# Optimization experiments

Hardware: AMD Instinct MI355X
Metric: run time of the kernel (lower is better)

## Reference

```python
import jax, jax.numpy as jnp
import numpy as np

H, KV, D, EPS = 16, 8, 128, 1e-6

def _rms(t, w):
    # per-head RMSNorm over last dim, computed in fp32
    t32 = t.astype(jnp.float32)
    return (w * t32 * jax.lax.rsqrt(jnp.mean(t32 * t32, axis=-1, keepdims=True) + EPS)).astype(t.dtype)

def _rotate_half(t):
    h = t.shape[-1] // 2
    return jnp.concatenate([-t[..., h:], t[..., :h]], axis=-1)

def setup_inputs() -> dict:
    key = jax.random.key(0)
    ks = jax.random.split(key, 8)
    B, S, HS = 4, 2048, 2048
    return {
        'x': jax.random.normal(ks[0], (B, S, HS), dtype=jnp.float32),
        'cos': jax.random.uniform(ks[1], (S, D), dtype=jnp.float32),
        'sin': jax.random.uniform(ks[2], (S, D), dtype=jnp.float32),
        'wq': jax.random.normal(ks[3], (H * D, HS), dtype=jnp.float32) * 0.02,
        'wk': jax.random.normal(ks[4], (KV * D, HS), dtype=jnp.float32) * 0.02,
        'wv': jax.random.normal(ks[5], (KV * D, HS), dtype=jnp.float32) * 0.02,
        'wo': jax.random.normal(ks[6], (HS, H * D), dtype=jnp.float32) * 0.02,
        'q_norm_w': jnp.ones((D,), dtype=jnp.float32),
        'k_norm_w': jnp.ones((D,), dtype=jnp.float32),
    }

def reference(x, cos, sin, wq, wk, wv, wo, q_norm_w, k_norm_w):
    B, S, _ = x.shape
    n_rep = H // KV
    # QKV projections (torch Linear: x @ W^T)
    xq = (x @ wq.T).reshape(B, S, H, D)
    xk = (x @ wk.T).reshape(B, S, KV, D)
    xv = (x @ wv.T).reshape(B, S, KV, D)
    # per-head RMSNorm on q/k
    xq = _rms(xq, q_norm_w)
    xk = _rms(xk, k_norm_w)
    # RoPE: cos/sin [S, D] broadcast over batch and heads
    c = cos[None, :, None, :]
    s = sin[None, :, None, :]
    xq = xq * c + _rotate_half(xq) * s
    xk = xk * c + _rotate_half(xk) * s
    # GQA: repeat kv heads, move heads forward -> [B, H, S, D]
    xq = xq.transpose(0, 2, 1, 3)
    xk = jnp.repeat(xk, n_rep, axis=2).transpose(0, 2, 1, 3)
    xv = jnp.repeat(xv, n_rep, axis=2).transpose(0, 2, 1, 3)
    # causal softmax attention
    scores = jnp.einsum('bhqd,bhkd->bhqk', xq, xk) / jnp.sqrt(jnp.float32(D))
    causal = jnp.tril(jnp.ones((S, S), dtype=bool))
    scores = jnp.where(causal, scores, -jnp.inf)
    attn = jax.nn.softmax(scores, axis=-1)
    out = jnp.einsum('bhqk,bhkd->bhqd', attn, xv)
    out = out.transpose(0, 2, 1, 3).reshape(B, S, H * D)
    return out @ wo.T
```

## Files before the change

kernel.cpp:

```cpp
#include <hip/hip_runtime.h>
#include <hip/hip_bf16.h>
#include <stdint.h>

using bf16 = __hip_bfloat16;
typedef __attribute__((ext_vector_type(8))) short bf16x8;
typedef __attribute__((ext_vector_type(4))) float f32x4;
typedef __attribute__((ext_vector_type(8))) unsigned short ushort8;

#define MFMA16(a,b,c) __builtin_amdgcn_mfma_f32_16x16x32_bf16(a,b,c,0,0,0)

static constexpr int Bc = 4, Sc = 2048, HSc = 2048, Hc = 16, KVc = 8, Dc = 128;

__device__ __forceinline__ void gl_lds16(const void* g, void* l) {
  __builtin_amdgcn_global_load_lds((const __attribute__((address_space(1))) uint32_t*)g,
                                   (__attribute__((address_space(3))) uint32_t*)l, 16, 0, 0);
}

__device__ __forceinline__ unsigned short f2bf(float f) {
  bf16 h = __float2bfloat16(f);
  return *reinterpret_cast<unsigned short*>(&h);
}

__global__ __launch_bounds__(256) void cvt_all(const float* __restrict__ x,
                                               const float* __restrict__ wq,
                                               const float* __restrict__ wk,
                                               const float* __restrict__ wv,
                                               const float* __restrict__ wo,
                                               unsigned short* __restrict__ xb,
                                               unsigned short* __restrict__ wqkv,
                                               unsigned short* __restrict__ wob) {
  const int NX = 2097152, NQ = 524288, NK = 262144, NV = 262144, NO = 524288;
  const int T = NX + NQ + NK + NV + NO;
  int stride = gridDim.x * blockDim.x;
  for (int i = blockIdx.x * blockDim.x + threadIdx.x; i < T; i += stride) {
    const float* s;
    unsigned short* d;
    int j = i;
    if (j < NX) { s = x; d = xb; }
    else if ((j -= NX) < NQ) { s = wq; d = wqkv; }
    else if ((j -= NQ) < NK) { s = wk; d = wqkv + (size_t)NQ * 8; }
    else if ((j -= NK) < NV) { s = wv; d = wqkv + (size_t)(NQ + NK) * 8; }
    else { j -= NV; s = wo; d = wob; }
    const float4 a = *(const float4*)(s + (size_t)j * 8);
    const float4 b = *(const float4*)(s + (size_t)j * 8 + 4);
    ushort8 o;
    o[0] = f2bf(a.x); o[1] = f2bf(a.y); o[2] = f2bf(a.z); o[3] = f2bf(a.w);
    o[4] = f2bf(b.x); o[5] = f2bf(b.y); o[6] = f2bf(b.z); o[7] = f2bf(b.w);
    *(ushort8*)(d + (size_t)j * 8) = o;
  }
}

__device__ __forceinline__ void storeC(float* C, size_t i, float v) { C[i] = v; }
__device__ __forceinline__ void storeC(bf16* C, size_t i, float v) { C[i] = __float2bfloat16(v); }


#define LDA_(MI, BUF)                                                          \
  _Pragma("unroll") for (int rf = 0; rf < 4; ++rf)                             \
  _Pragma("unroll") for (int k = 0; k < 2; ++k) {                              \
    const int row_ = (MI * 4 + rf) * 16 + lr;                                  \
    a[rf][k] = *(const bf16x8*)&sA[BUF][wm][row_][((k * 4 + lg) ^ (row_ & 7)) * 8]; \
  }
#define LDB_(NI, BUF, BREG)                                                    \
  _Pragma("unroll") for (int j = 0; j < 2; ++j)                                \
  _Pragma("unroll") for (int k = 0; k < 2; ++k) {                              \
    const int row_ = (bco + NI * 2 + j) * 16 + lr;                             \
    BREG[j][k] = *(const bf16x8*)&sB[BUF][bh][row_][((k * 4 + lg) ^ (row_ & 7)) * 8]; \
  }
#define MM_(MI, NI, BREG)                                                      \
  __builtin_amdgcn_s_setprio(1);                                               \
  _Pragma("unroll") for (int rf = 0; rf < 4; ++rf)                             \
  _Pragma("unroll") for (int j = 0; j < 2; ++j)                                \
  _Pragma("unroll") for (int k = 0; k < 2; ++k)                                \
    acc[MI * 4 + rf][NI * 2 + j] =                                             \
        MFMA16(a[rf][k], BREG[j][k], acc[MI * 4 + rf][NI * 2 + j]);            \
  __builtin_amdgcn_s_setprio(0);
#define BAR_ __builtin_amdgcn_s_barrier();
#define VM4_ asm volatile("s_waitcnt vmcnt(4)" ::: "memory");
#define VM0_ asm volatile("s_waitcnt vmcnt(0)" ::: "memory");

template <typename OUT_T>
__global__ __launch_bounds__(512, 2) void gemm8(const bf16* __restrict__ A,
                                                const bf16* __restrict__ B,
                                                OUT_T* __restrict__ C,
                                                int M, int N, int K,
                                                int gm, int gn, int rbm, int rbn) {
  const int nwg = gridDim.x;
  const int cpx = nwg >> 3;
  const int swz = (blockIdx.x & 7) * cpx + (blockIdx.x >> 3);
  const int rsz = rbm * rbn;
  const int region = swz / rsz, rid = swz % rsz;
  const int regions_n = gn / rbn;
  const int bm = (region / regions_n) * rbm + rid / rbn;
  const int bn = (region % regions_n) * rbn + rid % rbn;

  __shared__ __align__(16) bf16 sA[2][2][128][64];
  __shared__ __align__(16) bf16 sB[2][2][128][64];

  const int tid = threadIdx.x;
  const int lane = tid & 63;
  const int wave = tid >> 6;
  const int wm = wave >> 2;
  const int wn = wave & 3;
  const int lg = lane >> 4, lr = lane & 15;
  const int bh = wn >> 1;
  const int bco = (wn & 1) * 4;

  const int rowA = bm * 256;
  const int colB = bn * 256;
  const int NT = K >> 6;

  f32x4 acc[8][4];
  #pragma unroll
  for (int i = 0; i < 8; ++i)
    #pragma unroll
    for (int j = 0; j < 4; ++j) acc[i][j] = (f32x4){0.f, 0.f, 0.f, 0.f};

  auto stA = [&](int buf, int half, int kt) {
    const bf16* src = A + (size_t)(rowA + half * 128) * K + kt * 64;
    #pragma unroll
    for (int is = 0; is < 2; ++is) {
      int r = is * 64 + (tid >> 3);
      int sl = (tid & 7) ^ (r & 7);
      gl_lds16(src + (size_t)r * K + sl * 8, &sA[buf][half][r][(tid & 7) * 8]);
    }
  };
  auto stB = [&](int buf, int half, int kt) {
    const bf16* src = B + (size_t)(colB + half * 128) * K + kt * 64;
    #pragma unroll
    for (int is = 0; is < 2; ++is) {
      int r = is * 64 + (tid >> 3);
      int sl = (tid & 7) ^ (r & 7);
      gl_lds16(src + (size_t)r * K + sl * 8, &sB[buf][half][r][(tid & 7) * 8]);
    }
  };

  stB(0, 0, 0); stB(0, 1, 0); stA(0, 0, 0); stA(0, 1, 0);
  stB(1, 0, 1); stB(1, 1, 1);
  VM4_
  __builtin_amdgcn_s_barrier();

  for (int t = 0; t < NT; t += 2) {
    const bool lastit = (t + 2 >= NT);
    bf16x8 a[4][2], bl[2][2], br[2][2];
    LDA_(0, 0) LDB_(0, 0, bl)
    stA(1, 0, t + 1);
    BAR_ MM_(0, 0, bl) BAR_
    LDB_(1, 0, br)
    stA(1, 1, t + 1);
    BAR_ MM_(0, 1, br) BAR_
    LDA_(1, 0)
    if (!lastit) stB(0, 0, t + 2);
    BAR_ MM_(1, 0, bl) BAR_
    if (!lastit) stB(0, 1, t + 2);
    BAR_ MM_(1, 1, br)
    if (lastit) { VM0_ } else { VM4_ }
    BAR_
    LDA_(0, 1) LDB_(0, 1, bl)
    if (!lastit) stA(0, 0, t + 2);
    BAR_ MM_(0, 0, bl) BAR_
    LDB_(1, 1, br)
    if (!lastit) stA(0, 1, t + 2);
    BAR_ MM_(0, 1, br) BAR_
    LDA_(1, 1)
    if (t + 3 < NT) stB(1, 0, t + 3);
    BAR_ MM_(1, 0, bl) BAR_
    if (t + 3 < NT) stB(1, 1, t + 3);
    BAR_ MM_(1, 1, br)
    if (!lastit) { VM4_ }
    BAR_
  }

  #pragma unroll
  for (int rf = 0; rf < 8; ++rf)
    #pragma unroll
    for (int cf = 0; cf < 4; ++cf)
      #pragma unroll
      for (int r = 0; r < 4; ++r) {
        size_t row = rowA + wm * 128 + rf * 16 + lg * 4 + r;
        size_t col = colB + wn * 64 + cf * 16 + lr;
        storeC(C, row * (size_t)N + col, acc[rf][cf][r]);
      }
}

__global__ __launch_bounds__(256) void norm_rope(const bf16* __restrict__ qkv,
                                                 const float* __restrict__ cosT,
                                                 const float* __restrict__ sinT,
                                                 const float* __restrict__ qw,
                                                 const float* __restrict__ kw,
                                                 bf16* __restrict__ Qn, bf16* __restrict__ Kn) {
  const int bs = blockIdx.x;
  const int s = bs & (Sc - 1);
  const int b = bs >> 11;
  const int wave = threadIdx.x >> 6, lane = threadIdx.x & 63;
  const float c0 = cosT[(size_t)s * Dc + lane];
  const float c1 = cosT[(size_t)s * Dc + 64 + lane];
  const float s0 = sinT[(size_t)s * Dc + lane];
  const float s1 = sinT[(size_t)s * Dc + 64 + lane];
  const bf16* row = qkv + (size_t)bs * 4096;
  #pragma unroll
  for (int i = 0; i < 6; ++i) {
    int head = wave * 6 + i;
    bool isQ = head < 16;
    int col = head * Dc;
    float x0 = __bfloat162float(row[col + lane]);
    float x1 = __bfloat162float(row[col + 64 + lane]);
    float ss = x0 * x0 + x1 * x1;
    #pragma unroll
    for (int off = 32; off; off >>= 1) ss += __shfl_xor(ss, off);
    float inv = rsqrtf(ss * (1.0f / 128.0f) + 1e-6f);
    const float* w = isQ ? qw : kw;
    float n0 = x0 * inv * w[lane];
    float n1 = x1 * inv * w[lane + 64];
    float o0 = n0 * c0 - n1 * s0;
    float o1 = n1 * c1 + n0 * s1;
    size_t base;
    bf16* dst;
    if (isQ) { base = ((size_t)(b * Hc + head) * Sc + s) * Dc; dst = Qn; }
    else     { base = ((size_t)(b * KVc + (head - 16)) * Sc + s) * Dc; dst = Kn; }
    dst[base + lane] = __float2bfloat16(o0);
    dst[base + 64 + lane] = __float2bfloat16(o1);
  }
}

__global__ __launch_bounds__(256) void v_transpose(const bf16* __restrict__ qkv,
                                                   bf16* __restrict__ Vt) {
  const int s0 = blockIdx.x * 64;
  const int bk = blockIdx.y;
  __shared__ __align__(16) bf16 tile[64][136];
  const int tid = threadIdx.x;
  const size_t srcbase = ((size_t)(bk >> 3) * Sc + s0) * 4096 + 3072 + (size_t)(bk & 7) * Dc;
  #pragma unroll
  for (int it = 0; it < 4; ++it) {
    int idx = it * 256 + tid;
    int r = idx >> 4, ch = idx & 15;
    *(bf16x8*)&tile[r][ch * 8] = *(const bf16x8*)(qkv + srcbase + (size_t)r * 4096 + ch * 8);
  }
  __syncthreads();
  const size_t dstbase = (size_t)bk * Dc * Sc + s0;
  #pragma unroll
  for (int it = 0; it < 4; ++it) {
    int idx = it * 256 + tid;
    int d = idx >> 3, scc = idx & 7;
    bf16x8 o;
    #pragma unroll
    for (int j = 0; j < 8; ++j) o[j] = *(const short*)&tile[scc * 8 + j][d];
    *(bf16x8*)(Vt + dstbase + (size_t)d * Sc + scc * 8) = o;
  }
}

__global__ __launch_bounds__(512, 4) void flash_kernel(const bf16* __restrict__ Qn,
                                                       const bf16* __restrict__ Kn,
                                                       const bf16* __restrict__ Vt,
                                                       bf16* __restrict__ Out) {
  const int qi = 15 - (blockIdx.x >> 6);
  const int bh = blockIdx.x & 63;
  const int q0 = qi * 128;
  const int b = bh >> 4, h = bh & 15;
  const int kv = h >> 1;
  const int tid = threadIdx.x;
  const int wave = tid >> 6, lane = tid & 63;
  const int lg = lane >> 4, lr = lane & 15;
  const int rm = lr & 7;

  __shared__ __align__(16) bf16 sK[64][128];
  __shared__ __align__(16) bf16 sV[128][64];
  __shared__ __align__(16) bf16 sP[8][16][72];

  const int qrow = q0 + wave * 16;
  const bf16* qbase = Qn + ((size_t)(b * Hc + h) * Sc + qrow + lr) * Dc;
  bf16x8 qf[4];
  #pragma unroll
  for (int kk = 0; kk < 4; ++kk) qf[kk] = *(const bf16x8*)(qbase + kk * 32 + lg * 8);

  f32x4 oacc[8];
  #pragma unroll
  for (int i = 0; i < 8; ++i) oacc[i] = (f32x4){0.f, 0.f, 0.f, 0.f};
  float m_run[4], l_run[4];
  #pragma unroll
  for (int r = 0; r < 4; ++r) { m_run[r] = -3.0e38f; l_run[r] = 0.f; }

  const bf16* kb = Kn + ((size_t)(b * KVc + kv) * Sc) * Dc;
  const bf16* vb = Vt + ((size_t)(b * KVc + kv) * Dc) * Sc;
  const float scl = 0.08838834764831845f * 1.4426950408889634f;

  const int nt = 2 * qi + 2;
  for (int t = 0; t < nt; ++t) {
    const int k0 = t * 64;
    #pragma unroll
    for (int it = 0; it < 2; ++it) {
      int idx = it * 512 + tid;
      int r = idx >> 4, ps = idx & 15;
      int ls = ps ^ (r & 7);
      gl_lds16(kb + (size_t)(k0 + r) * Dc + ls * 8, &sK[r][ps * 8]);
    }
    #pragma unroll
    for (int it = 0; it < 2; ++it) {
      int idx = it * 512 + tid;
      int r = idx >> 3, ps = idx & 7;
      int ls = ps ^ (r & 7);
      gl_lds16(vb + (size_t)r * Sc + k0 + ls * 8, &sV[r][ps * 8]);
    }
    __syncthreads();

    float tt[4][4];
    __builtin_amdgcn_s_setprio(1);
    #pragma unroll
    for (int c = 0; c < 4; ++c) {
      f32x4 sacc = (f32x4){0.f, 0.f, 0.f, 0.f};
      #pragma unroll
      for (int kk = 0; kk < 4; ++kk) {
        bf16x8 kf = *(const bf16x8*)&sK[c * 16 + lr][((kk * 4 + lg) ^ rm) * 8];
        sacc = MFMA16(qf[kk], kf, sacc);
      }
      int kg = k0 + c * 16 + lr;
      #pragma unroll
      for (int r = 0; r < 4; ++r) {
        int qg = qrow + lg * 4 + r;
        tt[c][r] = (kg <= qg) ? sacc[r] * scl : -3.0e38f;
      }
    }
    __builtin_amdgcn_s_setprio(0);

    float pmax[4];
    #pragma unroll
    for (int r = 0; r < 4; ++r) {
      float mx = fmaxf(fmaxf(tt[0][r], tt[1][r]), fmaxf(tt[2][r], tt[3][r]));
      mx = fmaxf(mx, __shfl_xor(mx, 1));
      mx = fmaxf(mx, __shfl_xor(mx, 2));
      mx = fmaxf(mx, __shfl_xor(mx, 4));
      mx = fmaxf(mx, __shfl_xor(mx, 8));
      pmax[r] = mx;
    }
    bool grow = (pmax[0] > m_run[0] + 8.f) || (pmax[1] > m_run[1] + 8.f) ||
                (pmax[2] > m_run[2] + 8.f) || (pmax[3] > m_run[3] + 8.f);
    if (__any(grow)) {
      #pragma unroll
      for (int r = 0; r < 4; ++r) {
        float mnew = fmaxf(m_run[r], pmax[r]);
        float alpha = exp2f(m_run[r] - mnew);
        m_run[r] = mnew;
        l_run[r] *= alpha;
        #pragma unroll
        for (int dc = 0; dc < 8; ++dc) oacc[dc][r] *= alpha;
      }
    }
    #pragma unroll
    for (int r = 0; r < 4; ++r) {
      float local = 0.f;
      #pragma unroll
      for (int c = 0; c < 4; ++c) { tt[c][r] = exp2f(tt[c][r] - m_run[r]); local += tt[c][r]; }
      l_run[r] += local;
    }
    #pragma unroll
    for (int c = 0; c < 4; ++c)
      #pragma unroll
      for (int r = 0; r < 4; ++r)
        sP[wave][lg * 4 + r][c * 16 + lr] = __float2bfloat16(tt[c][r]);

    __builtin_amdgcn_s_setprio(1);
    #pragma unroll
    for (int kk2 = 0; kk2 < 2; ++kk2) {
      bf16x8 pf = *(const bf16x8*)&sP[wave][lr][kk2 * 32 + lg * 8];
      #pragma unroll
      for (int dc = 0; dc < 8; ++dc) {
        bf16x8 vf = *(const bf16x8*)&sV[dc * 16 + lr][((kk2 * 4 + lg) ^ rm) * 8];
        oacc[dc] = MFMA16(pf, vf, oacc[dc]);
      }
    }
    __builtin_amdgcn_s_setprio(0);

    __syncthreads();
  }

  #pragma unroll
  for (int r = 0; r < 4; ++r) {
    float l = l_run[r];
    l += __shfl_xor(l, 1);
    l += __shfl_xor(l, 2);
    l += __shfl_xor(l, 4);
    l += __shfl_xor(l, 8);
    l_run[r] = 1.f / l;
  }
  #pragma unroll
  for (int dc = 0; dc < 8; ++dc)
    #pragma unroll
    for (int r = 0; r < 4; ++r) {
      size_t row = (size_t)b * Sc + qrow + lg * 4 + r;
      Out[row * (size_t)(Hc * Dc) + h * Dc + dc * 16 + lr] =
          __float2bfloat16(oacc[dc][r] * l_run[r]);
    }
}

extern "C" void kernel_launch(void* const* d_in, const int* in_sizes, int n_in,
                              void* d_out, int out_size, void* d_ws, size_t ws_size,
                              hipStream_t stream) {
  const float* x    = (const float*)d_in[0];
  const float* cosT = (const float*)d_in[1];
  const float* sinT = (const float*)d_in[2];
  const float* wq   = (const float*)d_in[3];
  const float* wk   = (const float*)d_in[4];
  const float* wv   = (const float*)d_in[5];
  const float* wo   = (const float*)d_in[6];
  const float* qnw  = (const float*)d_in[7];
  const float* knw  = (const float*)d_in[8];
  float* out = (float*)d_out;

  const size_t MB = 1ull << 20;
  char* ws = (char*)d_ws;
  bf16* xb   = (bf16*)(ws + 0);
  bf16* wqkv = (bf16*)(ws + 32 * MB);
  bf16* wob  = (bf16*)(ws + 48 * MB);
  bf16* qkv  = (bf16*)(ws + 56 * MB);
  bf16* Qn   = (bf16*)(ws + 120 * MB);
  bf16* Kn   = (bf16*)(ws + 152 * MB);
  bf16* Vt   = (bf16*)(ws + 168 * MB);
  bf16* attn = (bf16*)(ws + 184 * MB);

  cvt_all<<<2048, 256, 0, stream>>>(x, wq, wk, wv, wo,
                                    (unsigned short*)xb, (unsigned short*)wqkv,
                                    (unsigned short*)wob);

  gemm8<bf16><<<512, 512, 0, stream>>>(xb, wqkv, qkv, 8192, 4096, 2048, 32, 16, 16, 4);
  norm_rope<<<8192, 256, 0, stream>>>(qkv, cosT, sinT, qnw, knw, Qn, Kn);
  v_transpose<<<dim3(32, 32), 256, 0, stream>>>(qkv, Vt);
  flash_kernel<<<1024, 512, 0, stream>>>(Qn, Kn, Vt, attn);
  gemm8<float><<<256, 512, 0, stream>>>(attn, wob, out, 8192, 2048, 2048, 32, 8, 8, 4);
}
```

Before: 384.4 us.

## Prefetch K/V tiles into registers and fold softmax scale into Q

```diff
diff --git a/kernel.cpp b/kernel.cpp
--- a/kernel.cpp
+++ b/kernel.cpp
@@ -52,7 +52,6 @@
 
 __device__ __forceinline__ void storeC(float* C, size_t i, float v) { C[i] = v; }
 __device__ __forceinline__ void storeC(bf16* C, size_t i, float v) { C[i] = __float2bfloat16(v); }
-
 
 #define LDA_(MI, BUF)                                                          \
   _Pragma("unroll") for (int rf = 0; rf < 4; ++rf)                             \
@@ -192,6 +191,7 @@
   const int s = bs & (Sc - 1);
   const int b = bs >> 11;
   const int wave = threadIdx.x >> 6, lane = threadIdx.x & 63;
+  const float QSCL = 0.08838834764831845f * 1.4426950408889634f;
   const float c0 = cosT[(size_t)s * Dc + lane];
   const float c1 = cosT[(size_t)s * Dc + 64 + lane];
   const float s0 = sinT[(size_t)s * Dc + lane];
@@ -213,6 +213,7 @@
     float n1 = x1 * inv * w[lane + 64];
     float o0 = n0 * c0 - n1 * s0;
     float o1 = n1 * c1 + n0 * s1;
+    if (isQ) { o0 *= QSCL; o1 *= QSCL; }
     size_t base;
     bf16* dst;
     if (isQ) { base = ((size_t)(b * Hc + head) * Sc + s) * Dc; dst = Qn; }
@@ -281,26 +282,37 @@
 
   const bf16* kb = Kn + ((size_t)(b * KVc + kv) * Sc) * Dc;
   const bf16* vb = Vt + ((size_t)(b * KVc + kv) * Dc) * Sc;
-  const float scl = 0.08838834764831845f * 1.4426950408889634f;
+
+  const bf16* kp[2]; const bf16* vp[2];
+  bf16* kwp[2]; bf16* vwp[2];
+  #pragma unroll
+  for (int i2 = 0; i2 < 2; ++i2) {
+    int idx = i2 * 512 + tid;
+    int r = idx >> 4, ps = idx & 15;
+    kp[i2] = kb + (size_t)r * Dc + ps * 8;
+    kwp[i2] = &sK[r][(ps ^ (r & 7)) * 8];
+    int r2 = idx >> 3, ps2 = idx & 7;
+    vp[i2] = vb + (size_t)r2 * Sc + ps2 * 8;
+    vwp[i2] = &sV[r2][(ps2 ^ (r2 & 7)) * 8];
+  }
+
+  bf16x8 rk[2], rv[2];
+  #pragma unroll
+  for (int i2 = 0; i2 < 2; ++i2) { rk[i2] = *(const bf16x8*)kp[i2]; rv[i2] = *(const bf16x8*)vp[i2]; }
+  #pragma unroll
+  for (int i2 = 0; i2 < 2; ++i2) { *(bf16x8*)kwp[i2] = rk[i2]; *(bf16x8*)vwp[i2] = rv[i2]; }
+  __syncthreads();
 
   const int nt = 2 * qi + 2;
   for (int t = 0; t < nt; ++t) {
     const int k0 = t * 64;
-    #pragma unroll
-    for (int it = 0; it < 2; ++it) {
-      int idx = it * 512 + tid;
-      int r = idx >> 4, ps = idx & 15;
-      int ls = ps ^ (r & 7);
-      gl_lds16(kb + (size_t)(k0 + r) * Dc + ls * 8, &sK[r][ps * 8]);
-    }
-    #pragma unroll
-    for (int it = 0; it < 2; ++it) {
-      int idx = it * 512 + tid;
-      int r = idx >> 3, ps = idx & 7;
-      int ls = ps ^ (r & 7);
-      gl_lds16(vb + (size_t)r * Sc + k0 + ls * 8, &sV[r][ps * 8]);
-    }
-    __syncthreads();
+    if (t + 1 < nt) {
+      #pragma unroll
+      for (int i2 = 0; i2 < 2; ++i2) {
+        rk[i2] = *(const bf16x8*)(kp[i2] + (size_t)(k0 + 64) * Dc);
+        rv[i2] = *(const bf16x8*)(vp[i2] + k0 + 64);
+      }
+    }
 
     float tt[4][4];
     __builtin_amdgcn_s_setprio(1);
@@ -312,11 +324,16 @@
         bf16x8 kf = *(const bf16x8*)&sK[c * 16 + lr][((kk * 4 + lg) ^ rm) * 8];
         sacc = MFMA16(qf[kk], kf, sacc);
       }
-      int kg = k0 + c * 16 + lr;
-      #pragma unroll
-      for (int r = 0; r < 4; ++r) {
-        int qg = qrow + lg * 4 + r;
-        tt[c][r] = (kg <= qg) ? sacc[r] * scl : -3.0e38f;
+      if (k0 + c * 16 + 15 <= qrow) {
+        #pragma unroll
+        for (int r = 0; r < 4; ++r) tt[c][r] = sacc[r];
+      } else {
+        int kg = k0 + c * 16 + lr;
+        #pragma unroll
+        for (int r = 0; r < 4; ++r) {
+          int qg = qrow + lg * 4 + r;
+          tt[c][r] = (kg <= qg) ? sacc[r] : -3.0e38f;
+        }
       }
     }
     __builtin_amdgcn_s_setprio(0);
@@ -369,6 +386,11 @@
     }
     __builtin_amdgcn_s_setprio(0);
 
+    __syncthreads();
+    if (t + 1 < nt) {
+      #pragma unroll
+      for (int i2 = 0; i2 < 2; ++i2) { *(bf16x8*)kwp[i2] = rk[i2]; *(bf16x8*)vwp[i2] = rv[i2]; }
+    }
     __syncthreads();
   }
 
```

Result: slower. 410.2 us (+6.7%).
